# Performance work log

Measured on AMD Instinct MI355X. Metric: run time of the kernel, lower is better.

Reference implementation:

```python
import jax, jax.numpy as jnp
import numpy as np

D_MODEL = 1024
NHEADS = 16
D_K = D_MODEL // NHEADS


def setup_inputs() -> dict:
    key = jax.random.key(0)
    ks = jax.random.split(key, 12)
    B, S = 2, 2048
    scale = 1.0 / np.sqrt(D_MODEL)
    inp = {
        "query": jax.random.normal(ks[0], (B, S, D_MODEL), dtype=jnp.float32),
        "key": jax.random.normal(ks[1], (B, S, D_MODEL), dtype=jnp.float32),
        "value": jax.random.normal(ks[2], (B, S, D_MODEL), dtype=jnp.float32),
        "mask": jax.random.randint(ks[3], (B, 1, S, S), 0, 2, dtype=jnp.int32),
        "Wq": jax.random.normal(ks[4], (D_MODEL, D_MODEL), dtype=jnp.float32) * scale,
        "bq": jnp.zeros((D_MODEL,), dtype=jnp.float32),
        "Wk": jax.random.normal(ks[5], (D_MODEL, D_MODEL), dtype=jnp.float32) * scale,
        "bk": jnp.zeros((D_MODEL,), dtype=jnp.float32),
        "Wv": jax.random.normal(ks[6], (D_MODEL, D_MODEL), dtype=jnp.float32) * scale,
        "bv": jnp.zeros((D_MODEL,), dtype=jnp.float32),
        "Wo": jax.random.normal(ks[7], (D_MODEL, D_MODEL), dtype=jnp.float32) * scale,
        "bo": jnp.zeros((D_MODEL,), dtype=jnp.float32),
    }
    return inp


def _split_heads(x):
    # [B, S, (H*D)] -> [B, H, S, D]
    B, S, _ = x.shape
    return x.reshape(B, S, NHEADS, D_K).transpose(0, 2, 1, 3)


def reference(query, key, value, mask, Wq, bq, Wk, bk, Wv, bv, Wo, bo):
    B, Sq, _ = query.shape
    q = _split_heads(query @ Wq + bq)            # [B, H, Sq, Dk]
    k = _split_heads(key @ Wk + bk)              # [B, H, Sk, Dk]
    v = _split_heads(value @ Wv + bv)            # [B, H, Sk, Dk]
    # scores: [B, H, Sq, Sk], scaled by sqrt(d_k)
    scores = jnp.einsum("bhqd,bhkd->bhqk", q, k) / np.sqrt(D_K).astype(np.float32)
    scores = jnp.where(mask == 0, jnp.float32(-1e12), scores)
    weights = jax.nn.softmax(scores, axis=-1)
    out = jnp.einsum("bhqk,bhkd->bhqd", weights, v)  # [B, H, Sq, Dk]
    out = out.transpose(0, 2, 1, 3).reshape(B, Sq, D_MODEL)
    return out @ Wo + bo  # dropout is identity in eval / p=0
```

## Files before the change

### kernel.cpp

```cpp
#include <hip/hip_runtime.h>
#include <math.h>

#define D_MODEL 1024
#define NHEADS  16
#define DK      64
#define BATCH   2
#define SEQ     2048
#define M_TOTAL (BATCH * SEQ)
#define CEXP    12.0f

typedef __attribute__((ext_vector_type(8))) short bf16x8;
typedef __attribute__((ext_vector_type(4))) float f32x4;

__device__ __forceinline__ unsigned short f2bf(float f) {
    union { float f; unsigned int i; } v; v.f = f;
    return (unsigned short)((v.i + 0x7FFFu + ((v.i >> 16) & 1u)) >> 16);
}

__device__ __forceinline__ void async_copy16(const void* g, void* l) {
    __builtin_amdgcn_global_load_lds(
        (const __attribute__((address_space(1))) unsigned int*)g,
        (__attribute__((address_space(3))) unsigned int*)l, 16, 0, 0);
}

struct Cvt3 { const float* s[3]; unsigned short* d[3]; };
__global__ __launch_bounds__(256)
void cvt_flat(const Cvt3 a)
{
    const float* __restrict__ s = a.s[blockIdx.z];
    unsigned short* __restrict__ d = a.d[blockIdx.z];
    const size_t i = ((size_t)blockIdx.x * 256 + threadIdx.x) * 4;
    const float4 v = *reinterpret_cast<const float4*>(&s[i]);
    ushort4 o;
    o.x = f2bf(v.x); o.y = f2bf(v.y); o.z = f2bf(v.z); o.w = f2bf(v.w);
    *reinterpret_cast<ushort4*>(&d[i]) = o;
}

struct Cvt4 { const float* s[4]; unsigned short* d[4]; };
__global__ __launch_bounds__(256)
void cvt_wt(const Cvt4 a)
{
    __shared__ unsigned short t[32][33];
    const float* __restrict__ W = a.s[blockIdx.z];
    unsigned short* __restrict__ WT = a.d[blockIdx.z];
    const int tx = threadIdx.x & 31;
    const int ty = threadIdx.x >> 5;
    const int nb = blockIdx.x << 5;
    const int kb = blockIdx.y << 5;
#pragma unroll
    for (int i = 0; i < 4; ++i)
        t[ty + (i << 3)][tx] = f2bf(W[(size_t)(kb + ty + (i << 3)) * D_MODEL + nb + tx]);
    __syncthreads();
#pragma unroll
    for (int i = 0; i < 4; ++i)
        WT[(size_t)(nb + ty + (i << 3)) * D_MODEL + kb + tx] = t[tx][ty + (i << 3)];
}

template <typename OutT> struct GArgs {
    const unsigned short* X[3];
    const unsigned short* W[3];
    const float*          Bi[3];
    OutT*                 O[3];
};

__device__ __forceinline__ void st_out(float* p, float v) { *p = v; }
__device__ __forceinline__ void st_out(unsigned short* p, float v) { *p = f2bf(v); }

template <typename OutT>
__global__ __launch_bounds__(256)
void gemm_bf16(const GArgs<OutT> args, const int head_split)
{
    __shared__ __align__(16) unsigned short As[128][32];
    __shared__ __align__(16) unsigned short Bs[128][32];

    const unsigned short* __restrict__ X  = args.X[blockIdx.z];
    const unsigned short* __restrict__ WT = args.W[blockIdx.z];
    const float* __restrict__ bias        = args.Bi[blockIdx.z];
    OutT* __restrict__ out                = args.O[blockIdx.z];

    const int tid = threadIdx.x;
    const int wid = tid >> 6;
    const int wy  = wid >> 1;
    const int wx  = wid & 1;
    const int l15 = tid & 15;
    const int kg  = (tid >> 4) & 3;
    const int n0  = blockIdx.x << 7;
    const int m0  = blockIdx.y << 7;

    const int lane = tid & 63;
    const int gr   = lane >> 2;
    const int gc   = (lane & 3) << 3;
    const int c0   = wid << 1;

    f32x4 acc[4][4];
#pragma unroll
    for (int i = 0; i < 4; ++i)
#pragma unroll
        for (int j = 0; j < 4; ++j)
            acc[i][j] = (f32x4){0.f, 0.f, 0.f, 0.f};

#pragma unroll 1
    for (int t = 0; t < D_MODEL / 32; ++t) {
        const int k0 = t << 5;

        __syncthreads();
#pragma unroll
        for (int cc = 0; cc < 2; ++cc) {
            const int c = c0 + cc;
            async_copy16(&X[(size_t)(m0 + (c << 4) + gr) * D_MODEL + k0 + gc],
                         &As[c << 4][0]);
            async_copy16(&WT[(size_t)(n0 + (c << 4) + gr) * D_MODEL + k0 + gc],
                         &Bs[c << 4][0]);
        }
        __syncthreads();

        bf16x8 a[4], b[4];
#pragma unroll
        for (int i = 0; i < 4; ++i)
            a[i] = *reinterpret_cast<const bf16x8*>(
                &As[(wy << 6) + (i << 4) + l15][kg << 3]);
#pragma unroll
        for (int j = 0; j < 4; ++j)
            b[j] = *reinterpret_cast<const bf16x8*>(
                &Bs[(wx << 6) + (j << 4) + l15][kg << 3]);
#pragma unroll
        for (int i = 0; i < 4; ++i)
#pragma unroll
            for (int j = 0; j < 4; ++j)
                acc[i][j] = __builtin_amdgcn_mfma_f32_16x16x32_bf16(
                    a[i], b[j], acc[i][j], 0, 0, 0);
    }

    float bv[4];
#pragma unroll
    for (int j = 0; j < 4; ++j)
        bv[j] = bias[n0 + (wx << 6) + (j << 4) + l15];

#pragma unroll
    for (int i = 0; i < 4; ++i) {
#pragma unroll
        for (int r = 0; r < 4; ++r) {
            const int m = m0 + (wy << 6) + (i << 4) + (kg << 2) + r;
#pragma unroll
            for (int j = 0; j < 4; ++j) {
                const int n = n0 + (wx << 6) + (j << 4) + l15;
                const float val = acc[i][j][r] + bv[j];
                if (head_split) {
                    const int bb = m >> 11;
                    const int ss = m & (SEQ - 1);
                    const int hh = n >> 6;
                    const int dd = n & (DK - 1);
                    st_out(&out[((size_t)(bb * NHEADS + hh) * SEQ + ss) * DK + dd], val);
                } else {
                    st_out(&out[(size_t)m * D_MODEL + n], val);
                }
            }
        }
    }
}

__global__ __launch_bounds__(256)
void flash_mfma(const unsigned short* __restrict__ Qb,
                const unsigned short* __restrict__ Kb,
                const unsigned short* __restrict__ Vb,
                const int* __restrict__ mask,
                unsigned short* __restrict__ ctx)
{
    __shared__ __align__(16) unsigned short Kbf[64][72];
    __shared__ __align__(16) unsigned short Vt [64][72];
    __shared__ __align__(16) unsigned short Pq [4][16][72];

    const int tid  = threadIdx.x;
    const int w    = tid >> 6;
    const int lane = tid & 63;
    const int l15  = lane & 15;
    const int kg   = lane >> 4;

    const int bb = blockIdx.z;
    const int hh = blockIdx.y;
    const int q0 = blockIdx.x << 6;

    const unsigned short* Qh = Qb + (size_t)(bb * NHEADS + hh) * SEQ * DK;
    const unsigned short* Kh = Kb + (size_t)(bb * NHEADS + hh) * SEQ * DK;
    const unsigned short* Vh = Vb + (size_t)(bb * NHEADS + hh) * SEQ * DK;

    bf16x8 aq[2];
    {
        const unsigned short* qrow = Qh + (size_t)(q0 + w * 16 + l15) * DK + (kg << 3);
        aq[0] = *reinterpret_cast<const bf16x8*>(qrow);
        aq[1] = *reinterpret_cast<const bf16x8*>(qrow + 32);
    }

    const int krow = tid >> 2;
    const int kcb  = (tid & 3) << 4;
    const int vkb  = (tid & 15) << 2;
    const int vdb  = (tid >> 4) << 2;

    const int* mbase = mask + ((size_t)bb * SEQ + (q0 + w * 16 + (kg << 2))) * SEQ + l15;

    float l_lane[4] = {0.f, 0.f, 0.f, 0.f};
    f32x4 O4[4];
#pragma unroll
    for (int n = 0; n < 4; ++n) O4[n] = (f32x4){0.f, 0.f, 0.f, 0.f};

#pragma unroll 1
    for (int t = 0; t < SEQ / 64; ++t) {
        const int k0 = t << 6;

        const uint4 kv0 = *reinterpret_cast<const uint4*>(
            Kh + (size_t)(k0 + krow) * DK + kcb);
        const uint4 kv1 = *reinterpret_cast<const uint4*>(
            Kh + (size_t)(k0 + krow) * DK + kcb + 8);
        uint2 vr[4];
#pragma unroll
        for (int i = 0; i < 4; ++i)
            vr[i] = *reinterpret_cast<const uint2*>(
                Vh + (size_t)(k0 + vkb + i) * DK + vdb);

        __syncthreads();
        *reinterpret_cast<uint4*>(&Kbf[krow][kcb])     = kv0;
        *reinterpret_cast<uint4*>(&Kbf[krow][kcb + 8]) = kv1;
        {
            uint2 o;
            o.x = (vr[0].x & 0xFFFFu) | (vr[1].x << 16);
            o.y = (vr[2].x & 0xFFFFu) | (vr[3].x << 16);
            *reinterpret_cast<uint2*>(&Vt[vdb + 0][vkb]) = o;
            o.x = (vr[0].x >> 16) | (vr[1].x & 0xFFFF0000u);
            o.y = (vr[2].x >> 16) | (vr[3].x & 0xFFFF0000u);
            *reinterpret_cast<uint2*>(&Vt[vdb + 1][vkb]) = o;
            o.x = (vr[0].y & 0xFFFFu) | (vr[1].y << 16);
            o.y = (vr[2].y & 0xFFFFu) | (vr[3].y << 16);
            *reinterpret_cast<uint2*>(&Vt[vdb + 2][vkb]) = o;
            o.x = (vr[0].y >> 16) | (vr[1].y & 0xFFFF0000u);
            o.y = (vr[2].y >> 16) | (vr[3].y & 0xFFFF0000u);
            *reinterpret_cast<uint2*>(&Vt[vdb + 3][vkb]) = o;
        }
        __syncthreads();

        int mv[4][4];
#pragma unroll
        for (int r = 0; r < 4; ++r)
#pragma unroll
            for (int n = 0; n < 4; ++n)
                mv[r][n] = mbase[(size_t)r * SEQ + k0 + 16 * n];

        f32x4 S[4];
#pragma unroll
        for (int n = 0; n < 4; ++n) {
            const bf16x8 b0 = *reinterpret_cast<const bf16x8*>(
                &Kbf[16 * n + l15][kg << 3]);
            const bf16x8 b1 = *reinterpret_cast<const bf16x8*>(
                &Kbf[16 * n + l15][(kg << 3) + 32]);
            f32x4 acc = (f32x4){0.f, 0.f, 0.f, 0.f};
            acc = __builtin_amdgcn_mfma_f32_16x16x32_bf16(aq[0], b0, acc, 0, 0, 0);
            acc = __builtin_amdgcn_mfma_f32_16x16x32_bf16(aq[1], b1, acc, 0, 0, 0);
            S[n] = acc;
        }

#pragma unroll
        for (int n = 0; n < 4; ++n)
#pragma unroll
            for (int r = 0; r < 4; ++r) {
                const float e = mv[r][n]
                    ? __expf(fmaf(S[n][r], 0.125f, -CEXP)) : 0.f;
                S[n][r] = e;
                l_lane[r] += e;
            }

#pragma unroll
        for (int r = 0; r < 4; ++r)
#pragma unroll
            for (int n = 0; n < 4; ++n)
                Pq[w][(kg << 2) + r][16 * n + l15] = f2bf(S[n][r]);

        __asm__ volatile("s_waitcnt lgkmcnt(0)" ::: "memory");

        const bf16x8 ap0 = *reinterpret_cast<const bf16x8*>(&Pq[w][l15][kg << 3]);
        const bf16x8 ap1 = *reinterpret_cast<const bf16x8*>(&Pq[w][l15][(kg << 3) + 32]);
#pragma unroll
        for (int n = 0; n < 4; ++n) {
            const bf16x8 b0 = *reinterpret_cast<const bf16x8*>(
                &Vt[16 * n + l15][kg << 3]);
            const bf16x8 b1 = *reinterpret_cast<const bf16x8*>(
                &Vt[16 * n + l15][(kg << 3) + 32]);
            O4[n] = __builtin_amdgcn_mfma_f32_16x16x32_bf16(ap0, b0, O4[n], 0, 0, 0);
            O4[n] = __builtin_amdgcn_mfma_f32_16x16x32_bf16(ap1, b1, O4[n], 0, 0, 0);
        }
    }

#pragma unroll
    for (int r = 0; r < 4; ++r) {
        float rsum = l_lane[r];
        rsum += __shfl_xor(rsum, 1);
        rsum += __shfl_xor(rsum, 2);
        rsum += __shfl_xor(rsum, 4);
        rsum += __shfl_xor(rsum, 8);
        const float inv = 1.f / rsum;
        const size_t base =
            (size_t)(bb * SEQ + q0 + w * 16 + (kg << 2) + r) * D_MODEL + hh * DK + l15;
#pragma unroll
        for (int n = 0; n < 4; ++n)
            ctx[base + 16 * n] = f2bf(O4[n][r] * inv);
    }
}

extern "C" void kernel_launch(void* const* d_in, const int* in_sizes, int n_in,
                              void* d_out, int out_size, void* d_ws, size_t ws_size,
                              hipStream_t stream)
{
    const float* query = (const float*)d_in[0];
    const float* key   = (const float*)d_in[1];
    const float* value = (const float*)d_in[2];
    const int*   mask  = (const int*)d_in[3];
    const float* Wq = (const float*)d_in[4];
    const float* bq = (const float*)d_in[5];
    const float* Wk = (const float*)d_in[6];
    const float* bk = (const float*)d_in[7];
    const float* Wv = (const float*)d_in[8];
    const float* bv = (const float*)d_in[9];
    const float* Wo = (const float*)d_in[10];
    const float* bo = (const float*)d_in[11];

    unsigned short* ws = (unsigned short*)d_ws;
    const size_t TE = (size_t)M_TOTAL * D_MODEL;
    const size_t WE = (size_t)D_MODEL * D_MODEL;
    unsigned short* Xq  = ws;
    unsigned short* Xk  = Xq + TE;
    unsigned short* Xv  = Xk + TE;
    unsigned short* WTq = Xv + TE;
    unsigned short* WTk = WTq + WE;
    unsigned short* WTv = WTk + WE;
    unsigned short* WTo = WTv + WE;
    unsigned short* Qb  = WTo + WE;
    unsigned short* Kb  = Qb + TE;
    unsigned short* Vb  = Kb + TE;
    unsigned short* Ctx = Vb + TE;

    Cvt3 c3;
    c3.s[0] = query; c3.s[1] = key; c3.s[2] = value;
    c3.d[0] = Xq;    c3.d[1] = Xk;  c3.d[2] = Xv;
    cvt_flat<<<dim3(TE / 1024, 1, 3), 256, 0, stream>>>(c3);

    Cvt4 c4;
    c4.s[0] = Wq;  c4.s[1] = Wk;  c4.s[2] = Wv;  c4.s[3] = Wo;
    c4.d[0] = WTq; c4.d[1] = WTk; c4.d[2] = WTv; c4.d[3] = WTo;
    cvt_wt<<<dim3(32, 32, 4), 256, 0, stream>>>(c4);

    GArgs<unsigned short> qkv;
    qkv.X[0] = Xq;  qkv.X[1] = Xk;  qkv.X[2] = Xv;
    qkv.W[0] = WTq; qkv.W[1] = WTk; qkv.W[2] = WTv;
    qkv.Bi[0] = bq; qkv.Bi[1] = bk; qkv.Bi[2] = bv;
    qkv.O[0] = Qb;  qkv.O[1] = Kb;  qkv.O[2] = Vb;
    gemm_bf16<unsigned short><<<dim3(8, 32, 3), 256, 0, stream>>>(qkv, 1);

    flash_mfma<<<dim3(SEQ / 64, NHEADS, BATCH), 256, 0, stream>>>(
        Qb, Kb, Vb, mask, Ctx);

    GArgs<float> op;
    op.X[0] = Ctx;  op.X[1] = Ctx;  op.X[2] = Ctx;
    op.W[0] = WTo;  op.W[1] = WTo;  op.W[2] = WTo;
    op.Bi[0] = bo;  op.Bi[1] = bo;  op.Bi[2] = bo;
    op.O[0] = (float*)d_out; op.O[1] = (float*)d_out; op.O[2] = (float*)d_out;
    gemm_bf16<float><<<dim3(8, 32, 1), 256, 0, stream>>>(op, 0);
}
```

Measured before the change: 310.0 us.

## Pack mask into wave ballot bitmasks, prefetch K/V, use raw exp2 softmax

Adds a pre-pass kernel that packs the int32 mask into 64-bit per-wave ballot words laid out by the flash kernel's MFMA fragments. The attention kernel then reads 16 scalar words per tile instead of 16 int loads per lane, which removes heavy re-reading of the full mask across all 16 heads. It also software-prefetches the next K/V tile into registers, replaces expf with v_exp_f32 using pre-scaled log2e constants plus cndmask and a hardware bf16 convert, and swizzles GEMM block order to improve L2 locality. The costs are an extra launch, extra workspace, and more register pressure from the prefetch.

```diff
diff --git a/kernel.cpp b/kernel.cpp
--- a/kernel.cpp
+++ b/kernel.cpp
@@ -7,7 +7,9 @@
 #define BATCH   2
 #define SEQ     2048
 #define M_TOTAL (BATCH * SEQ)
-#define CEXP    12.0f
+#define NT      (SEQ / 64)
+#define CK1 0.18033688011112042f
+#define CK0 -17.312340490667561f
 
 typedef __attribute__((ext_vector_type(8))) short bf16x8;
 typedef __attribute__((ext_vector_type(4))) float f32x4;
@@ -56,6 +58,33 @@
         WT[(size_t)(nb + ty + (i << 3)) * D_MODEL + kb + tx] = t[tx][ty + (i << 3)];
 }
 
+__global__ __launch_bounds__(256)
+void mask_pack(const int* __restrict__ mask, unsigned long long* __restrict__ wm)
+{
+    const int tid  = threadIdx.x;
+    const int lane = tid & 63;
+    const int l15  = lane & 15;
+    const int kg   = lane >> 4;
+    const int wv   = ((int)blockIdx.x << 2) + (tid >> 6);
+    const int t    = wv & 31;
+    const int qw   = (wv >> 5) & 127;
+    const int bb   = wv >> 12;
+
+    const int* mb = mask + (size_t)bb * SEQ * SEQ;
+    const int qrow = (qw << 4) + (kg << 2);
+    const int kcol = (t << 6) + l15;
+    unsigned long long* wout = wm + ((((size_t)bb * 128 + qw) * 32 + t) << 4);
+
+#pragma unroll
+    for (int r = 0; r < 4; ++r)
+#pragma unroll
+        for (int n = 0; n < 4; ++n) {
+            const int m = mb[(size_t)(qrow + r) * SEQ + kcol + (n << 4)];
+            const unsigned long long bal = __ballot(m != 0);
+            if (lane == 0) wout[(r << 2) | n] = bal;
+        }
+}
+
 template <typename OutT> struct GArgs {
     const unsigned short* X[3];
     const unsigned short* W[3];
@@ -84,8 +113,11 @@
     const int wx  = wid & 1;
     const int l15 = tid & 15;
     const int kg  = (tid >> 4) & 3;
-    const int n0  = blockIdx.x << 7;
-    const int m0  = blockIdx.y << 7;
+
+    const int id = ((int)blockIdx.y << 3) | (int)blockIdx.x;
+    const int sw = ((id & 7) << 5) | (id >> 3);
+    const int n0 = (sw & 7) << 7;
+    const int m0 = (sw >> 3) << 7;
 
     const int lane = tid & 63;
     const int gr   = lane >> 2;
@@ -146,11 +178,11 @@
                 const int n = n0 + (wx << 6) + (j << 4) + l15;
                 const float val = acc[i][j][r] + bv[j];
                 if (head_split) {
-                    const int bb = m >> 11;
-                    const int ss = m & (SEQ - 1);
-                    const int hh = n >> 6;
-                    const int dd = n & (DK - 1);
-                    st_out(&out[((size_t)(bb * NHEADS + hh) * SEQ + ss) * DK + dd], val);
+                    const int bbx = m >> 11;
+                    const int ss  = m & (SEQ - 1);
+                    const int hhx = n >> 6;
+                    const int dd  = n & (DK - 1);
+                    st_out(&out[((size_t)(bbx * NHEADS + hhx) * SEQ + ss) * DK + dd], val);
                 } else {
                     st_out(&out[(size_t)m * D_MODEL + n], val);
                 }
@@ -163,7 +195,7 @@
 void flash_mfma(const unsigned short* __restrict__ Qb,
                 const unsigned short* __restrict__ Kb,
                 const unsigned short* __restrict__ Vb,
-                const int* __restrict__ mask,
+                const unsigned long long* __restrict__ wmask,
                 unsigned short* __restrict__ ctx)
 {
     __shared__ __align__(16) unsigned short Kbf[64][72];
@@ -196,27 +228,23 @@
     const int vkb  = (tid & 15) << 2;
     const int vdb  = (tid >> 4) << 2;
 
-    const int* mbase = mask + ((size_t)bb * SEQ + (q0 + w * 16 + (kg << 2))) * SEQ + l15;
+    const int wbase = __builtin_amdgcn_readfirstlane(
+        (bb * 128 + (q0 >> 4) + w) << 9);
 
     float l_lane[4] = {0.f, 0.f, 0.f, 0.f};
     f32x4 O4[4];
 #pragma unroll
     for (int n = 0; n < 4; ++n) O4[n] = (f32x4){0.f, 0.f, 0.f, 0.f};
 
+    uint4 kv0 = *reinterpret_cast<const uint4*>(Kh + (size_t)krow * DK + kcb);
+    uint4 kv1 = *reinterpret_cast<const uint4*>(Kh + (size_t)krow * DK + kcb + 8);
+    uint2 vr[4];
+#pragma unroll
+    for (int i = 0; i < 4; ++i)
+        vr[i] = *reinterpret_cast<const uint2*>(Vh + (size_t)(vkb + i) * DK + vdb);
+
 #pragma unroll 1
-    for (int t = 0; t < SEQ / 64; ++t) {
-        const int k0 = t << 6;
-
-        const uint4 kv0 = *reinterpret_cast<const uint4*>(
-            Kh + (size_t)(k0 + krow) * DK + kcb);
-        const uint4 kv1 = *reinterpret_cast<const uint4*>(
-            Kh + (size_t)(k0 + krow) * DK + kcb + 8);
-        uint2 vr[4];
-#pragma unroll
-        for (int i = 0; i < 4; ++i)
-            vr[i] = *reinterpret_cast<const uint2*>(
-                Vh + (size_t)(k0 + vkb + i) * DK + vdb);
-
+    for (int t = 0; t < NT; ++t) {
         __syncthreads();
         *reinterpret_cast<uint4*>(&Kbf[krow][kcb])     = kv0;
         *reinterpret_cast<uint4*>(&Kbf[krow][kcb + 8]) = kv1;
@@ -237,12 +265,20 @@
         }
         __syncthreads();
 
-        int mv[4][4];
-#pragma unroll
-        for (int r = 0; r < 4; ++r)
-#pragma unroll
-            for (int n = 0; n < 4; ++n)
-                mv[r][n] = mbase[(size_t)r * SEQ + k0 + 16 * n];
+        if (t + 1 < NT) {
+            const int kn = (t + 1) << 6;
+            kv0 = *reinterpret_cast<const uint4*>(Kh + (size_t)(kn + krow) * DK + kcb);
+            kv1 = *reinterpret_cast<const uint4*>(Kh + (size_t)(kn + krow) * DK + kcb + 8);
+#pragma unroll
+            for (int i = 0; i < 4; ++i)
+                vr[i] = *reinterpret_cast<const uint2*>(
+                    Vh + (size_t)(kn + vkb + i) * DK + vdb);
+        }
+
+        const unsigned long long* wmt = wmask + wbase + (t << 4);
+        unsigned long long wmv[16];
+#pragma unroll
+        for (int rn = 0; rn < 16; ++rn) wmv[rn] = wmt[rn];
 
         f32x4 S[4];
 #pragma unroll
@@ -261,17 +297,16 @@
         for (int n = 0; n < 4; ++n)
 #pragma unroll
             for (int r = 0; r < 4; ++r) {
-                const float e = mv[r][n]
-                    ? __expf(fmaf(S[n][r], 0.125f, -CEXP)) : 0.f;
-                S[n][r] = e;
-                l_lane[r] += e;
+                float x = fmaf(S[n][r], CK1, CK0);
+                __asm__("v_exp_f32 %0, %1" : "=v"(x) : "v"(x));
+                __asm__("v_cndmask_b32 %0, 0, %1, %2"
+                        : "=v"(x) : "v"(x), "s"(wmv[(r << 2) | n]));
+                l_lane[r] += x;
+                unsigned pk;
+                __asm__("v_cvt_pk_bf16_f32 %0, %1, %2"
+                        : "=v"(pk) : "v"(x), "v"(x));
+                Pq[w][(kg << 2) + r][16 * n + l15] = (unsigned short)pk;
             }
-
-#pragma unroll
-        for (int r = 0; r < 4; ++r)
-#pragma unroll
-            for (int n = 0; n < 4; ++n)
-                Pq[w][(kg << 2) + r][16 * n + l15] = f2bf(S[n][r]);
 
         __asm__ volatile("s_waitcnt lgkmcnt(0)" ::: "memory");
 
@@ -335,6 +370,7 @@
     unsigned short* Kb  = Qb + TE;
     unsigned short* Vb  = Kb + TE;
     unsigned short* Ctx = Vb + TE;
+    unsigned long long* WM = (unsigned long long*)(Ctx + TE);
 
     Cvt3 c3;
     c3.s[0] = query; c3.s[1] = key; c3.s[2] = value;
@@ -345,6 +381,8 @@
     c4.s[0] = Wq;  c4.s[1] = Wk;  c4.s[2] = Wv;  c4.s[3] = Wo;
     c4.d[0] = WTq; c4.d[1] = WTk; c4.d[2] = WTv; c4.d[3] = WTo;
     cvt_wt<<<dim3(32, 32, 4), 256, 0, stream>>>(c4);
+
+    mask_pack<<<dim3(2048, 1, 1), 256, 0, stream>>>(mask, WM);
 
     GArgs<unsigned short> qkv;
     qkv.X[0] = Xq;  qkv.X[1] = Xk;  qkv.X[2] = Xv;
@@ -354,7 +392,7 @@
     gemm_bf16<unsigned short><<<dim3(8, 32, 3), 256, 0, stream>>>(qkv, 1);
 
     flash_mfma<<<dim3(SEQ / 64, NHEADS, BATCH), 256, 0, stream>>>(
-        Qb, Kb, Vb, mask, Ctx);
+        Qb, Kb, Vb, WM, Ctx);
 
     GArgs<float> op;
     op.X[0] = Ctx;  op.X[1] = Ctx;  op.X[2] = Ctx;
```

New measurement: 298.1 us. 3.8% less time.
